# Performance work log

Hardware: AMD Instinct MI355X
Metric: run time of the kernel (lower is better)

## Reference

```python
import jax, jax.numpy as jnp
import numpy as np

T, B, D, H = 256, 4096, 128, 16


def setup_inputs() -> dict:
    key = jax.random.key(0)
    ks = jax.random.split(key, 6)
    feat = jax.random.normal(ks[0], (T, B, D), dtype=jnp.float32)
    # begin-of-episode mask in {0,1}; resets hidden state where 1
    begin_mask = jax.random.randint(ks[1], (T, B, 1), 0, 2).astype(jnp.float32)
    hx0 = jnp.zeros((B, H), dtype=jnp.float32)
    s = 1.0 / np.sqrt(H)  # torch GRUCell default init: U(-1/sqrt(H), 1/sqrt(H))
    W_ih = jax.random.uniform(ks[2], (3 * H, D), jnp.float32, -s, s)
    W_hh = jax.random.uniform(ks[3], (3 * H, H), jnp.float32, -s, s)
    b_ih = jax.random.uniform(ks[4], (3 * H,), jnp.float32, -s, s)
    b_hh = jax.random.uniform(ks[5], (3 * H,), jnp.float32, -s, s)
    return dict(feat=feat, begin_mask=begin_mask, hx0=hx0,
                W_ih=W_ih, W_hh=W_hh, b_ih=b_ih, b_hh=b_hh)


def reference(feat, begin_mask, hx0, W_ih, W_hh, b_ih, b_hh):
    # feat: [T,B,D]; begin_mask: [T,B,1]; hx0: [B,H]
    # torch GRUCell gate order along the 3H axis: r, z, n
    h_dim = hx0.shape[-1]
    # Input projections are state-independent -> one big batched GEMM upfront.
    gx = jnp.einsum('tbd,gd->tbg', feat, W_ih) + b_ih  # [T,B,3H]

    def step(h, inp):
        gx_t, m_t = inp                      # [B,3H], [B,1]
        h = h * (1.0 - m_t)                  # begin-mask reset
        gh = h @ W_hh.T + b_hh               # [B,3H]
        r = jax.nn.sigmoid(gx_t[:, :h_dim] + gh[:, :h_dim])
        z = jax.nn.sigmoid(gx_t[:, h_dim:2 * h_dim] + gh[:, h_dim:2 * h_dim])
        n = jnp.tanh(gx_t[:, 2 * h_dim:] + r * gh[:, 2 * h_dim:])
        h = (1.0 - z) * n + z * h
        return h, h

    _, output = jax.lax.scan(step, hx0, (gx, begin_mask))  # output: [T,B,H]
    # original returns (output, {'hx': output}) -- same stacked tensor
    return output
```

## Files before the change

kernel.cpp:

```cpp
#include <hip/hip_runtime.h>
#include <cstdint>


#define TT 256
#define BB 4096
#define DD 128
#define HH 16
#define TC 4
#define NCH (TT / TC)
#define EPB 16

typedef float    f32x4  __attribute__((ext_vector_type(4)));
typedef short    bf16x8 __attribute__((ext_vector_type(8)));
typedef uint32_t u32x4  __attribute__((ext_vector_type(4)));

__global__ __launch_bounds__(256, 1) void gru_fused(
    const float* __restrict__ feat, const float* __restrict__ bmask,
    const float* __restrict__ hx0, const float* __restrict__ Wih,
    const float* __restrict__ Whh, const float* __restrict__ bih,
    const float* __restrict__ bhh, float* __restrict__ out) {
  __shared__ __align__(16) float As[4][TC * EPB * DD];
  __shared__ __align__(16) float ms[4][256];

  const int tid  = threadIdx.x;
  const int lane = tid & 63;
  const int wv   = tid >> 6;
  const int li   = lane & 15;
  const int lq   = lane >> 4;
  const int b0   = blockIdx.x * EPB;
  const int si   = li;
  const int se   = wv * 4 + lq;

  auto stage = [&](int c) {
    char* AsB = (char*)As[c & 3];
    char* msB = (char*)ms[c & 3] + wv * 256;
    const char* base =
        (const char*)(feat + (size_t)c * TC * BB * DD + (size_t)b0 * DD);
#pragma unroll
    for (int k = 0; k < 8; ++k) {
      int s = wv * 8 + k;
      int row = 2 * s + (lane >> 5);
      int e = row >> 2, tq = row & 3;
      int inrow = (lane & 31) << 4;
      int off = e * (DD * 4) + (inrow ^ ((row & 7) << 4));
      const char* g = base + (size_t)tq * ((size_t)BB * DD * 4) + off;
      __builtin_amdgcn_global_load_lds(
          (const __attribute__((address_space(1))) void*)g,
          (__attribute__((address_space(3))) void*)(AsB + s * 1024), 16, 0, 0);
    }
    {
      int tq = lane & 3, el = (lane >> 2) & 3;
      const char* g =
          (const char*)(bmask + (size_t)(c * TC + tq) * BB + b0 + wv * 4 + el);
      __builtin_amdgcn_global_load_lds(
          (const __attribute__((address_space(1))) void*)g,
          (__attribute__((address_space(3))) void*)msB, 4, 0, 0);
    }
  };

  bf16x8 Bh[4][3], Bl[4][3];
#pragma unroll
  for (int ks = 0; ks < 4; ++ks)
#pragma unroll
    for (int n = 0; n < 3; ++n) {
      const char* wp =
          (const char*)Wih + (16 * n + li) * 512 + ks * 128 + lq * 32;
      f32x4 w0 = *(const f32x4*)wp;
      f32x4 w1 = *(const f32x4*)(wp + 16);
      float wsv[8] = {w0.x, w0.y, w0.z, w0.w, w1.x, w1.y, w1.z, w1.w};
      uint32_t hiw[4], low[4];
#pragma unroll
      for (int j2 = 0; j2 < 4; ++j2) {
        uint32_t e0 = __float_as_uint(wsv[2 * j2]);
        uint32_t e1 = __float_as_uint(wsv[2 * j2 + 1]);
        uint32_t h0 = e0 & 0xFFFF0000u, h1 = e1 & 0xFFFF0000u;
        hiw[j2] = (h0 >> 16) | h1;
        float l0 = wsv[2 * j2] - __uint_as_float(h0);
        float l1 = wsv[2 * j2 + 1] - __uint_as_float(h1);
        low[j2] = (__float_as_uint(l0) >> 16) |
                  (__float_as_uint(l1) & 0xFFFF0000u);
      }
      Bh[ks][n] = __builtin_bit_cast(bf16x8, (u32x4){hiw[0], hiw[1], hiw[2], hiw[3]});
      Bl[ks][n] = __builtin_bit_cast(bf16x8, (u32x4){low[0], low[1], low[2], low[3]});
    }

  float whhA[16], whhB[16], whhC[16];
#pragma unroll
  for (int j = 0; j < 16; ++j) {
    whhA[j] = Whh[si * HH + j];
    whhB[j] = Whh[(si + 16) * HH + j];
    whhC[j] = Whh[(si + 32) * HH + j];
  }
  const float bhA = bhh[si], bhB = bhh[si + 16], bhC = bhh[si + 32];
  const float biA = bih[si], biB = bih[si + 16], biC = bih[si + 32];
  float h = hx0[(size_t)(b0 + se) * HH + si];

  stage(0);
  stage(1);
  stage(2);
  stage(3);

  const int pbase = (lane & 48) << 2;

  for (int c = 0; c < NCH; ++c) {
    if (c == 0)            asm volatile("s_waitcnt vmcnt(27)" ::: "memory");
    else if (c == 1)       asm volatile("s_waitcnt vmcnt(31)" ::: "memory");
    else if (c == 2)       asm volatile("s_waitcnt vmcnt(35)" ::: "memory");
    else if (c == 3)       asm volatile("s_waitcnt vmcnt(39)" ::: "memory");
    else if (c == NCH - 3) asm volatile("s_waitcnt vmcnt(34)" ::: "memory");
    else if (c == NCH - 2) asm volatile("s_waitcnt vmcnt(25)" ::: "memory");
    else if (c == NCH - 1) asm volatile("s_waitcnt vmcnt(16)" ::: "memory");
    else                   asm volatile("s_waitcnt vmcnt(43)" ::: "memory");

    f32x4 mm = *(const f32x4*)((const char*)ms[c & 3] + wv * 256 + lq * 16);

    const char* AsB = (const char*)As[c & 3];
    f32x4 acc0 = {0.f, 0.f, 0.f, 0.f};
    f32x4 acc1 = {0.f, 0.f, 0.f, 0.f};
    f32x4 acc2 = {0.f, 0.f, 0.f, 0.f};
#pragma unroll
    for (int ks = 0; ks < 4; ++ks) {
      int row = wv * 16 + li;
      int a0o = row * 512 + ((ks * 128 + lq * 32) ^ ((row & 7) << 4));
      f32x4 x0 = *(const f32x4*)(AsB + a0o);
      f32x4 x1 = *(const f32x4*)(AsB + (a0o ^ 16));
      float xs[8] = {x0.x, x0.y, x0.z, x0.w, x1.x, x1.y, x1.z, x1.w};
      uint32_t hiw[4], low[4];
#pragma unroll
      for (int j2 = 0; j2 < 4; ++j2) {
        uint32_t e0 = __float_as_uint(xs[2 * j2]);
        uint32_t e1 = __float_as_uint(xs[2 * j2 + 1]);
        uint32_t h0 = e0 & 0xFFFF0000u, h1 = e1 & 0xFFFF0000u;
        hiw[j2] = (h0 >> 16) | h1;
        float l0 = xs[2 * j2] - __uint_as_float(h0);
        float l1 = xs[2 * j2 + 1] - __uint_as_float(h1);
        low[j2] = (__float_as_uint(l0) >> 16) |
                  (__float_as_uint(l1) & 0xFFFF0000u);
      }
      bf16x8 Ah = __builtin_bit_cast(bf16x8, (u32x4){hiw[0], hiw[1], hiw[2], hiw[3]});
      bf16x8 Al = __builtin_bit_cast(bf16x8, (u32x4){low[0], low[1], low[2], low[3]});
      acc0 = __builtin_amdgcn_mfma_f32_16x16x32_bf16(Ah, Bh[ks][0], acc0, 0, 0, 0);
      acc0 = __builtin_amdgcn_mfma_f32_16x16x32_bf16(Al, Bh[ks][0], acc0, 0, 0, 0);
      acc0 = __builtin_amdgcn_mfma_f32_16x16x32_bf16(Ah, Bl[ks][0], acc0, 0, 0, 0);
      acc1 = __builtin_amdgcn_mfma_f32_16x16x32_bf16(Ah, Bh[ks][1], acc1, 0, 0, 0);
      acc1 = __builtin_amdgcn_mfma_f32_16x16x32_bf16(Al, Bh[ks][1], acc1, 0, 0, 0);
      acc1 = __builtin_amdgcn_mfma_f32_16x16x32_bf16(Ah, Bl[ks][1], acc1, 0, 0, 0);
      acc2 = __builtin_amdgcn_mfma_f32_16x16x32_bf16(Ah, Bh[ks][2], acc2, 0, 0, 0);
      acc2 = __builtin_amdgcn_mfma_f32_16x16x32_bf16(Al, Bh[ks][2], acc2, 0, 0, 0);
      acc2 = __builtin_amdgcn_mfma_f32_16x16x32_bf16(Ah, Bl[ks][2], acc2, 0, 0, 0);
    }

    if (c + 4 < NCH) stage(c + 4);

#pragma unroll
    for (int tq = 0; tq < 4; ++tq) {
      float f = 1.0f - mm[tq];
      float d0 = 0.f, d1 = 0.f, d2 = 0.f;
#pragma unroll
      for (int j = 0; j < 16; ++j) {
        float hj = __uint_as_float((uint32_t)__builtin_amdgcn_ds_bpermute(
            pbase + 4 * j, (int)__float_as_uint(h)));
        d0 = __builtin_fmaf(whhA[j], hj, d0);
        d1 = __builtin_fmaf(whhB[j], hj, d1);
        d2 = __builtin_fmaf(whhC[j], hj, d2);
      }
      float g0 = acc0[tq] + biA;
      float g1 = acc1[tq] + biB;
      float g2 = acc2[tq] + biC;
      float r = 1.0f / (1.0f + __expf(-(g0 + f * d0 + bhA)));
      float z = 1.0f / (1.0f + __expf(-(g1 + f * d1 + bhB)));
      float a = g2 + r * (f * d2 + bhC);
      float n = 2.0f / (1.0f + __expf(-2.0f * a)) - 1.0f;
      float hm = f * h;
      h = n + z * (hm - n);
      out[((size_t)(c * TC + tq) * BB + b0 + se) * HH + si] = h;
    }
  }
}

extern "C" void kernel_launch(void* const* d_in, const int* in_sizes, int n_in,
                              void* d_out, int out_size, void* d_ws,
                              size_t ws_size, hipStream_t stream) {
  const float* feat  = (const float*)d_in[0];
  const float* bmask = (const float*)d_in[1];
  const float* hx0   = (const float*)d_in[2];
  const float* Wih   = (const float*)d_in[3];
  const float* Whh   = (const float*)d_in[4];
  const float* bih   = (const float*)d_in[5];
  const float* bhh   = (const float*)d_in[6];
  float* out = (float*)d_out;
  gru_fused<<<dim3(BB / EPB), dim3(256), 0, stream>>>(feat, bmask, hx0, Wih,
                                                      Whh, bih, bhh, out);
}
```

Measured before the change: 192.8 us.

## Replace LDS staging with register double-buffered global prefetch of features

Drops the shared-memory ring that async global-to-LDS loads filled, along with its hand-tuned vmcnt waits. Each lane now loads its own MFMA A-fragment rows and mask values straight into registers, two chunks ahead, using ping-pong register buffers. This removes the LDS write and read traffic and the swizzle arithmetic. In exchange it needs many more VGPRs, has a shallower prefetch depth (2 chunks instead of 4), and leaves the compiler to insert the waits, which may be conservative.

Result: slower. 234.7 us (+21.7%).

```diff
diff --git a/kernel.cpp b/kernel.cpp
--- a/kernel.cpp
+++ b/kernel.cpp
@@ -14,14 +14,29 @@
 typedef short    bf16x8 __attribute__((ext_vector_type(8)));
 typedef uint32_t u32x4  __attribute__((ext_vector_type(4)));
 
+__device__ __forceinline__ void split8(const f32x4& x0, const f32x4& x1,
+                                       bf16x8& hi8, bf16x8& lo8) {
+  float xs[8] = {x0.x, x0.y, x0.z, x0.w, x1.x, x1.y, x1.z, x1.w};
+  uint32_t hiw[4], low[4];
+#pragma unroll
+  for (int j = 0; j < 4; ++j) {
+    uint32_t e0 = __float_as_uint(xs[2 * j]);
+    uint32_t e1 = __float_as_uint(xs[2 * j + 1]);
+    uint32_t h0 = e0 & 0xFFFF0000u, h1 = e1 & 0xFFFF0000u;
+    hiw[j] = (h0 >> 16) | h1;
+    float l0 = xs[2 * j] - __uint_as_float(h0);
+    float l1 = xs[2 * j + 1] - __uint_as_float(h1);
+    low[j] = (__float_as_uint(l0) >> 16) | (__float_as_uint(l1) & 0xFFFF0000u);
+  }
+  hi8 = __builtin_bit_cast(bf16x8, (u32x4){hiw[0], hiw[1], hiw[2], hiw[3]});
+  lo8 = __builtin_bit_cast(bf16x8, (u32x4){low[0], low[1], low[2], low[3]});
+}
+
 __global__ __launch_bounds__(256, 1) void gru_fused(
     const float* __restrict__ feat, const float* __restrict__ bmask,
     const float* __restrict__ hx0, const float* __restrict__ Wih,
     const float* __restrict__ Whh, const float* __restrict__ bih,
     const float* __restrict__ bhh, float* __restrict__ out) {
-  __shared__ __align__(16) float As[4][TC * EPB * DD];
-  __shared__ __align__(16) float ms[4][256];
-
   const int tid  = threadIdx.x;
   const int lane = tid & 63;
   const int wv   = tid >> 6;
@@ -31,32 +46,29 @@
   const int si   = li;
   const int se   = wv * 4 + lq;
 
-  auto stage = [&](int c) {
-    char* AsB = (char*)As[c & 3];
-    char* msB = (char*)ms[c & 3] + wv * 256;
+  const int tqA = li & 3;
+  const int eA  = wv * 4 + (li >> 2);
+  const size_t rowByte = (size_t)tqA * ((size_t)BB * DD * 4) +
+                         (size_t)(b0 + eA) * (DD * 4) + (size_t)lq * 32;
+
+  auto issue = [&](int c, f32x4 (&pa)[8], float (&pm)[4]) {
     const char* base =
-        (const char*)(feat + (size_t)c * TC * BB * DD + (size_t)b0 * DD);
+        (const char*)feat + (size_t)c * ((size_t)TC * BB * DD * 4) + rowByte;
 #pragma unroll
-    for (int k = 0; k < 8; ++k) {
-      int s = wv * 8 + k;
-      int row = 2 * s + (lane >> 5);
-      int e = row >> 2, tq = row & 3;
-      int inrow = (lane & 31) << 4;
-      int off = e * (DD * 4) + (inrow ^ ((row & 7) << 4));
-      const char* g = base + (size_t)tq * ((size_t)BB * DD * 4) + off;
-      __builtin_amdgcn_global_load_lds(
-          (const __attribute__((address_space(1))) void*)g,
-          (__attribute__((address_space(3))) void*)(AsB + s * 1024), 16, 0, 0);
+    for (int ks = 0; ks < 4; ++ks) {
+      pa[2 * ks]     = *(const f32x4*)(base + ks * 128);
+      pa[2 * ks + 1] = *(const f32x4*)(base + ks * 128 + 16);
     }
-    {
-      int tq = lane & 3, el = (lane >> 2) & 3;
-      const char* g =
-          (const char*)(bmask + (size_t)(c * TC + tq) * BB + b0 + wv * 4 + el);
-      __builtin_amdgcn_global_load_lds(
-          (const __attribute__((address_space(1))) void*)g,
-          (__attribute__((address_space(3))) void*)msB, 4, 0, 0);
-    }
+#pragma unroll
+    for (int t2 = 0; t2 < 4; ++t2)
+      pm[t2] = bmask[(size_t)(c * TC + t2) * BB + b0 + se];
   };
+
+  f32x4 paA[8], paB[8];
+  float pmA[4], pmB[4];
+  issue(0, paA, pmA);
+  issue(1, paB, pmB);
+  asm volatile("" ::: "memory");
 
   bf16x8 Bh[4][3], Bl[4][3];
 #pragma unroll
@@ -67,21 +79,7 @@
           (const char*)Wih + (16 * n + li) * 512 + ks * 128 + lq * 32;
       f32x4 w0 = *(const f32x4*)wp;
       f32x4 w1 = *(const f32x4*)(wp + 16);
-      float wsv[8] = {w0.x, w0.y, w0.z, w0.w, w1.x, w1.y, w1.z, w1.w};
-      uint32_t hiw[4], low[4];
-#pragma unroll
-      for (int j2 = 0; j2 < 4; ++j2) {
-        uint32_t e0 = __float_as_uint(wsv[2 * j2]);
-        uint32_t e1 = __float_as_uint(wsv[2 * j2 + 1]);
-        uint32_t h0 = e0 & 0xFFFF0000u, h1 = e1 & 0xFFFF0000u;
-        hiw[j2] = (h0 >> 16) | h1;
-        float l0 = wsv[2 * j2] - __uint_as_float(h0);
-        float l1 = wsv[2 * j2 + 1] - __uint_as_float(h1);
-        low[j2] = (__float_as_uint(l0) >> 16) |
-                  (__float_as_uint(l1) & 0xFFFF0000u);
-      }
-      Bh[ks][n] = __builtin_bit_cast(bf16x8, (u32x4){hiw[0], hiw[1], hiw[2], hiw[3]});
-      Bl[ks][n] = __builtin_bit_cast(bf16x8, (u32x4){low[0], low[1], low[2], low[3]});
+      split8(w0, w1, Bh[ks][n], Bl[ks][n]);
     }
 
   float whhA[16], whhB[16], whhC[16];
@@ -95,50 +93,17 @@
   const float biA = bih[si], biB = bih[si + 16], biC = bih[si + 32];
   float h = hx0[(size_t)(b0 + se) * HH + si];
 
-  stage(0);
-  stage(1);
-  stage(2);
-  stage(3);
-
   const int pbase = (lane & 48) << 2;
 
-  for (int c = 0; c < NCH; ++c) {
-    if (c == 0)            asm volatile("s_waitcnt vmcnt(27)" ::: "memory");
-    else if (c == 1)       asm volatile("s_waitcnt vmcnt(31)" ::: "memory");
-    else if (c == 2)       asm volatile("s_waitcnt vmcnt(35)" ::: "memory");
-    else if (c == 3)       asm volatile("s_waitcnt vmcnt(39)" ::: "memory");
-    else if (c == NCH - 3) asm volatile("s_waitcnt vmcnt(34)" ::: "memory");
-    else if (c == NCH - 2) asm volatile("s_waitcnt vmcnt(25)" ::: "memory");
-    else if (c == NCH - 1) asm volatile("s_waitcnt vmcnt(16)" ::: "memory");
-    else                   asm volatile("s_waitcnt vmcnt(43)" ::: "memory");
-
-    f32x4 mm = *(const f32x4*)((const char*)ms[c & 3] + wv * 256 + lq * 16);
-
-    const char* AsB = (const char*)As[c & 3];
+  auto body = [&](int c, f32x4 (&pa)[8], float (&pm)[4]) {
+    float m0 = pm[0], m1 = pm[1], m2 = pm[2], m3 = pm[3];
     f32x4 acc0 = {0.f, 0.f, 0.f, 0.f};
     f32x4 acc1 = {0.f, 0.f, 0.f, 0.f};
     f32x4 acc2 = {0.f, 0.f, 0.f, 0.f};
 #pragma unroll
     for (int ks = 0; ks < 4; ++ks) {
-      int row = wv * 16 + li;
-      int a0o = row * 512 + ((ks * 128 + lq * 32) ^ ((row & 7) << 4));
-      f32x4 x0 = *(const f32x4*)(AsB + a0o);
-      f32x4 x1 = *(const f32x4*)(AsB + (a0o ^ 16));
-      float xs[8] = {x0.x, x0.y, x0.z, x0.w, x1.x, x1.y, x1.z, x1.w};
-      uint32_t hiw[4], low[4];
-#pragma unroll
-      for (int j2 = 0; j2 < 4; ++j2) {
-        uint32_t e0 = __float_as_uint(xs[2 * j2]);
-        uint32_t e1 = __float_as_uint(xs[2 * j2 + 1]);
-        uint32_t h0 = e0 & 0xFFFF0000u, h1 = e1 & 0xFFFF0000u;
-        hiw[j2] = (h0 >> 16) | h1;
-        float l0 = xs[2 * j2] - __uint_as_float(h0);
-        float l1 = xs[2 * j2 + 1] - __uint_as_float(h1);
-        low[j2] = (__float_as_uint(l0) >> 16) |
-                  (__float_as_uint(l1) & 0xFFFF0000u);
-      }
-      bf16x8 Ah = __builtin_bit_cast(bf16x8, (u32x4){hiw[0], hiw[1], hiw[2], hiw[3]});
-      bf16x8 Al = __builtin_bit_cast(bf16x8, (u32x4){low[0], low[1], low[2], low[3]});
+      bf16x8 Ah, Al;
+      split8(pa[2 * ks], pa[2 * ks + 1], Ah, Al);
       acc0 = __builtin_amdgcn_mfma_f32_16x16x32_bf16(Ah, Bh[ks][0], acc0, 0, 0, 0);
       acc0 = __builtin_amdgcn_mfma_f32_16x16x32_bf16(Al, Bh[ks][0], acc0, 0, 0, 0);
       acc0 = __builtin_amdgcn_mfma_f32_16x16x32_bf16(Ah, Bl[ks][0], acc0, 0, 0, 0);
@@ -149,9 +114,10 @@
       acc2 = __builtin_amdgcn_mfma_f32_16x16x32_bf16(Al, Bh[ks][2], acc2, 0, 0, 0);
       acc2 = __builtin_amdgcn_mfma_f32_16x16x32_bf16(Ah, Bl[ks][2], acc2, 0, 0, 0);
     }
+    if (c + 2 < NCH) issue(c + 2, pa, pm);
+    asm volatile("" ::: "memory");
 
-    if (c + 4 < NCH) stage(c + 4);
-
+    float mm[4] = {m0, m1, m2, m3};
 #pragma unroll
     for (int tq = 0; tq < 4; ++tq) {
       float f = 1.0f - mm[tq];
@@ -175,6 +141,11 @@
       h = n + z * (hm - n);
       out[((size_t)(c * TC + tq) * BB + b0 + se) * HH + si] = h;
     }
+  };
+
+  for (int cc = 0; cc < NCH; cc += 2) {
+    body(cc, paA, pmA);
+    body(cc + 1, paB, pmB);
   }
 }
 
```

## Split loads onto dedicated producer waves and pack recurrent FMAs into f32x2

Applied to the files above, without the earlier changes.

Adds four producer waves per block that stream feature and mask chunks into LDS via global_load_lds, synchronizing with the four compute waves through per-chunk s_barrier. This removes load-issue and vmcnt waits from the compute critical path and allows two blocks per CU. The recurrent h@W_hh dot product now uses packed two-wide FMAs. The costs are an extra barrier per chunk, a shallower prefetch depth and more register pressure under the tighter launch bounds.

After: 189.5 us. Within noise of the previous version (-1.7%).

```diff
diff --git a/kernel.cpp b/kernel.cpp
--- a/kernel.cpp
+++ b/kernel.cpp
@@ -10,11 +10,30 @@
 #define NCH (TT / TC)
 #define EPB 16
 
+typedef float    f32x2  __attribute__((ext_vector_type(2)));
 typedef float    f32x4  __attribute__((ext_vector_type(4)));
 typedef short    bf16x8 __attribute__((ext_vector_type(8)));
 typedef uint32_t u32x4  __attribute__((ext_vector_type(4)));
 
-__global__ __launch_bounds__(256, 1) void gru_fused(
+__device__ __forceinline__ void split8(const f32x4& x0, const f32x4& x1,
+                                       bf16x8& hi8, bf16x8& lo8) {
+  float xs[8] = {x0.x, x0.y, x0.z, x0.w, x1.x, x1.y, x1.z, x1.w};
+  uint32_t hiw[4], low[4];
+#pragma unroll
+  for (int j = 0; j < 4; ++j) {
+    uint32_t e0 = __float_as_uint(xs[2 * j]);
+    uint32_t e1 = __float_as_uint(xs[2 * j + 1]);
+    uint32_t h0 = e0 & 0xFFFF0000u, h1 = e1 & 0xFFFF0000u;
+    hiw[j] = (h0 >> 16) | h1;
+    float l0 = xs[2 * j] - __uint_as_float(h0);
+    float l1 = xs[2 * j + 1] - __uint_as_float(h1);
+    low[j] = (__float_as_uint(l0) >> 16) | (__float_as_uint(l1) & 0xFFFF0000u);
+  }
+  hi8 = __builtin_bit_cast(bf16x8, (u32x4){hiw[0], hiw[1], hiw[2], hiw[3]});
+  lo8 = __builtin_bit_cast(bf16x8, (u32x4){low[0], low[1], low[2], low[3]});
+}
+
+__global__ __launch_bounds__(512, 2) void gru_fused(
     const float* __restrict__ feat, const float* __restrict__ bmask,
     const float* __restrict__ hx0, const float* __restrict__ Wih,
     const float* __restrict__ Whh, const float* __restrict__ bih,
@@ -25,38 +44,56 @@
   const int tid  = threadIdx.x;
   const int lane = tid & 63;
   const int wv   = tid >> 6;
-  const int li   = lane & 15;
-  const int lq   = lane >> 4;
   const int b0   = blockIdx.x * EPB;
-  const int si   = li;
-  const int se   = wv * 4 + lq;
 
-  auto stage = [&](int c) {
-    char* AsB = (char*)As[c & 3];
-    char* msB = (char*)ms[c & 3] + wv * 256;
-    const char* base =
-        (const char*)(feat + (size_t)c * TC * BB * DD + (size_t)b0 * DD);
+  if (wv >= 4) {
+    const int hw = wv - 4;
+    auto stage = [&](int c) {
+      char* AsB = (char*)As[c & 3];
+      char* msB = (char*)ms[c & 3] + hw * 256;
+      const char* base =
+          (const char*)(feat + (size_t)c * TC * BB * DD + (size_t)b0 * DD);
 #pragma unroll
-    for (int k = 0; k < 8; ++k) {
-      int s = wv * 8 + k;
-      int row = 2 * s + (lane >> 5);
-      int e = row >> 2, tq = row & 3;
-      int inrow = (lane & 31) << 4;
-      int off = e * (DD * 4) + (inrow ^ ((row & 7) << 4));
-      const char* g = base + (size_t)tq * ((size_t)BB * DD * 4) + off;
-      __builtin_amdgcn_global_load_lds(
-          (const __attribute__((address_space(1))) void*)g,
-          (__attribute__((address_space(3))) void*)(AsB + s * 1024), 16, 0, 0);
+      for (int k = 0; k < 8; ++k) {
+        int s = hw * 8 + k;
+        int row = 2 * s + (lane >> 5);
+        int e = row >> 2, tq = row & 3;
+        int inrow = (lane & 31) << 4;
+        int off = e * (DD * 4) + (inrow ^ ((row & 7) << 4));
+        const char* g = base + (size_t)tq * ((size_t)BB * DD * 4) + off;
+        __builtin_amdgcn_global_load_lds(
+            (const __attribute__((address_space(1))) void*)g,
+            (__attribute__((address_space(3))) void*)(AsB + s * 1024), 16, 0, 0);
+      }
+      {
+        int tq = lane & 3, el = (lane >> 2) & 3;
+        const char* g = (const char*)(bmask + (size_t)(c * TC + tq) * BB + b0 +
+                                      hw * 4 + el);
+        __builtin_amdgcn_global_load_lds(
+            (const __attribute__((address_space(1))) void*)g,
+            (__attribute__((address_space(3))) void*)msB, 4, 0, 0);
+      }
+    };
+    stage(0);
+    stage(1);
+    stage(2);
+    asm volatile("s_waitcnt vmcnt(18)" ::: "memory");
+    for (int c = 0; c < NCH; ++c) {
+      __builtin_amdgcn_s_barrier();
+      asm volatile("" ::: "memory");
+      if (c + 3 < NCH) stage(c + 3);
+      if (c <= NCH - 4)      asm volatile("s_waitcnt vmcnt(18)" ::: "memory");
+      else if (c == NCH - 3) asm volatile("s_waitcnt vmcnt(9)" ::: "memory");
+      else if (c == NCH - 2) asm volatile("s_waitcnt vmcnt(0)" ::: "memory");
+      asm volatile("" ::: "memory");
     }
-    {
-      int tq = lane & 3, el = (lane >> 2) & 3;
-      const char* g =
-          (const char*)(bmask + (size_t)(c * TC + tq) * BB + b0 + wv * 4 + el);
-      __builtin_amdgcn_global_load_lds(
-          (const __attribute__((address_space(1))) void*)g,
-          (__attribute__((address_space(3))) void*)msB, 4, 0, 0);
-    }
-  };
+    return;
+  }
+
+  const int li = lane & 15;
+  const int lq = lane >> 4;
+  const int si = li;
+  const int se = wv * 4 + lq;
 
   bf16x8 Bh[4][3], Bl[4][3];
 #pragma unroll
@@ -67,50 +104,26 @@
           (const char*)Wih + (16 * n + li) * 512 + ks * 128 + lq * 32;
       f32x4 w0 = *(const f32x4*)wp;
       f32x4 w1 = *(const f32x4*)(wp + 16);
-      float wsv[8] = {w0.x, w0.y, w0.z, w0.w, w1.x, w1.y, w1.z, w1.w};
-      uint32_t hiw[4], low[4];
-#pragma unroll
-      for (int j2 = 0; j2 < 4; ++j2) {
-        uint32_t e0 = __float_as_uint(wsv[2 * j2]);
-        uint32_t e1 = __float_as_uint(wsv[2 * j2 + 1]);
-        uint32_t h0 = e0 & 0xFFFF0000u, h1 = e1 & 0xFFFF0000u;
-        hiw[j2] = (h0 >> 16) | h1;
-        float l0 = wsv[2 * j2] - __uint_as_float(h0);
-        float l1 = wsv[2 * j2 + 1] - __uint_as_float(h1);
-        low[j2] = (__float_as_uint(l0) >> 16) |
-                  (__float_as_uint(l1) & 0xFFFF0000u);
-      }
-      Bh[ks][n] = __builtin_bit_cast(bf16x8, (u32x4){hiw[0], hiw[1], hiw[2], hiw[3]});
-      Bl[ks][n] = __builtin_bit_cast(bf16x8, (u32x4){low[0], low[1], low[2], low[3]});
+      split8(w0, w1, Bh[ks][n], Bl[ks][n]);
     }
 
-  float whhA[16], whhB[16], whhC[16];
+  f32x2 whhA2[8], whhB2[8], whhC2[8];
 #pragma unroll
-  for (int j = 0; j < 16; ++j) {
-    whhA[j] = Whh[si * HH + j];
-    whhB[j] = Whh[(si + 16) * HH + j];
-    whhC[j] = Whh[(si + 32) * HH + j];
+  for (int k = 0; k < 8; ++k) {
+    whhA2[k] = *(const f32x2*)&Whh[si * HH + 2 * k];
+    whhB2[k] = *(const f32x2*)&Whh[(si + 16) * HH + 2 * k];
+    whhC2[k] = *(const f32x2*)&Whh[(si + 32) * HH + 2 * k];
   }
   const float bhA = bhh[si], bhB = bhh[si + 16], bhC = bhh[si + 32];
   const float biA = bih[si], biB = bih[si + 16], biC = bih[si + 32];
   float h = hx0[(size_t)(b0 + se) * HH + si];
 
-  stage(0);
-  stage(1);
-  stage(2);
-  stage(3);
-
   const int pbase = (lane & 48) << 2;
 
   for (int c = 0; c < NCH; ++c) {
-    if (c == 0)            asm volatile("s_waitcnt vmcnt(27)" ::: "memory");
-    else if (c == 1)       asm volatile("s_waitcnt vmcnt(31)" ::: "memory");
-    else if (c == 2)       asm volatile("s_waitcnt vmcnt(35)" ::: "memory");
-    else if (c == 3)       asm volatile("s_waitcnt vmcnt(39)" ::: "memory");
-    else if (c == NCH - 3) asm volatile("s_waitcnt vmcnt(34)" ::: "memory");
-    else if (c == NCH - 2) asm volatile("s_waitcnt vmcnt(25)" ::: "memory");
-    else if (c == NCH - 1) asm volatile("s_waitcnt vmcnt(16)" ::: "memory");
-    else                   asm volatile("s_waitcnt vmcnt(43)" ::: "memory");
+    asm volatile("" ::: "memory");
+    __builtin_amdgcn_s_barrier();
+    asm volatile("" ::: "memory");
 
     f32x4 mm = *(const f32x4*)((const char*)ms[c & 3] + wv * 256 + lq * 16);
 
@@ -124,21 +137,8 @@
       int a0o = row * 512 + ((ks * 128 + lq * 32) ^ ((row & 7) << 4));
       f32x4 x0 = *(const f32x4*)(AsB + a0o);
       f32x4 x1 = *(const f32x4*)(AsB + (a0o ^ 16));
-      float xs[8] = {x0.x, x0.y, x0.z, x0.w, x1.x, x1.y, x1.z, x1.w};
-      uint32_t hiw[4], low[4];
-#pragma unroll
-      for (int j2 = 0; j2 < 4; ++j2) {
-        uint32_t e0 = __float_as_uint(xs[2 * j2]);
-        uint32_t e1 = __float_as_uint(xs[2 * j2 + 1]);
-        uint32_t h0 = e0 & 0xFFFF0000u, h1 = e1 & 0xFFFF0000u;
-        hiw[j2] = (h0 >> 16) | h1;
-        float l0 = xs[2 * j2] - __uint_as_float(h0);
-        float l1 = xs[2 * j2 + 1] - __uint_as_float(h1);
-        low[j2] = (__float_as_uint(l0) >> 16) |
-                  (__float_as_uint(l1) & 0xFFFF0000u);
-      }
-      bf16x8 Ah = __builtin_bit_cast(bf16x8, (u32x4){hiw[0], hiw[1], hiw[2], hiw[3]});
-      bf16x8 Al = __builtin_bit_cast(bf16x8, (u32x4){low[0], low[1], low[2], low[3]});
+      bf16x8 Ah, Al;
+      split8(x0, x1, Ah, Al);
       acc0 = __builtin_amdgcn_mfma_f32_16x16x32_bf16(Ah, Bh[ks][0], acc0, 0, 0, 0);
       acc0 = __builtin_amdgcn_mfma_f32_16x16x32_bf16(Al, Bh[ks][0], acc0, 0, 0, 0);
       acc0 = __builtin_amdgcn_mfma_f32_16x16x32_bf16(Ah, Bl[ks][0], acc0, 0, 0, 0);
@@ -150,20 +150,24 @@
       acc2 = __builtin_amdgcn_mfma_f32_16x16x32_bf16(Ah, Bl[ks][2], acc2, 0, 0, 0);
     }
 
-    if (c + 4 < NCH) stage(c + 4);
-
 #pragma unroll
     for (int tq = 0; tq < 4; ++tq) {
       float f = 1.0f - mm[tq];
-      float d0 = 0.f, d1 = 0.f, d2 = 0.f;
+      f32x2 dA = {0.f, 0.f}, dB = {0.f, 0.f}, dC = {0.f, 0.f};
 #pragma unroll
-      for (int j = 0; j < 16; ++j) {
-        float hj = __uint_as_float((uint32_t)__builtin_amdgcn_ds_bpermute(
-            pbase + 4 * j, (int)__float_as_uint(h)));
-        d0 = __builtin_fmaf(whhA[j], hj, d0);
-        d1 = __builtin_fmaf(whhB[j], hj, d1);
-        d2 = __builtin_fmaf(whhC[j], hj, d2);
+      for (int k = 0; k < 8; ++k) {
+        float hx = __uint_as_float((uint32_t)__builtin_amdgcn_ds_bpermute(
+            pbase + 8 * k, (int)__float_as_uint(h)));
+        float hy = __uint_as_float((uint32_t)__builtin_amdgcn_ds_bpermute(
+            pbase + 8 * k + 4, (int)__float_as_uint(h)));
+        f32x2 hp = {hx, hy};
+        dA = __builtin_elementwise_fma(whhA2[k], hp, dA);
+        dB = __builtin_elementwise_fma(whhB2[k], hp, dB);
+        dC = __builtin_elementwise_fma(whhC2[k], hp, dC);
       }
+      float d0 = dA.x + dA.y;
+      float d1 = dB.x + dB.y;
+      float d2 = dC.x + dC.y;
       float g0 = acc0[tq] + biA;
       float g1 = acc1[tq] + biB;
       float g2 = acc2[tq] + biC;
@@ -189,6 +193,6 @@
   const float* bih   = (const float*)d_in[5];
   const float* bhh   = (const float*)d_in[6];
   float* out = (float*)d_out;
-  gru_fused<<<dim3(BB / EPB), dim3(256), 0, stream>>>(feat, bmask, hx0, Wih,
+  gru_fused<<<dim3(BB / EPB), dim3(512), 0, stream>>>(feat, bmask, hx0, Wih,
                                                       Whh, bih, bhh, out);
 }
```
